# Kernel optimization log

Hardware: AMD Instinct MI355X
Metric: run time of the kernel (lower is better)

The kernel has to match this reference:

```python
import jax, jax.numpy as jnp
import numpy as np

B = 256          # batch
H = 1024         # conditioning_size (dec_hid_dim)
D = 256          # gst_dim
G = 32           # num_gst
C = 16           # num_cells
O = 256          # output_size


def setup_inputs() -> dict:
    key = jax.random.key(0)
    ks = jax.random.split(key, 7)
    hidden = jax.random.normal(ks[0], (B, H), dtype=jnp.float32)
    # per-cell embedding tables: nn.Embedding(num_gst, gst_dim) stacked over cells
    gst_emb = jax.random.normal(ks[1], (C, G, D), dtype=jnp.float32)
    # per-cell Linear(gst_dim + cond, cond): weight [H, H + D] (torch [out, in]), bias [H]
    attn_w = jax.random.normal(ks[2], (C, H, H + D), dtype=jnp.float32) * 0.02
    attn_b = jax.random.normal(ks[3], (C, H), dtype=jnp.float32) * 0.02
    # per-cell v: Parameter(torch.rand(cond))
    v = jax.random.uniform(ks[4], (C, H), dtype=jnp.float32)
    # out Linear(gst_dim, output_size)
    out_w = jax.random.normal(ks[5], (O, D), dtype=jnp.float32) * 0.02
    out_b = jax.random.normal(ks[6], (O,), dtype=jnp.float32) * 0.02
    return {"hidden": hidden, "gst_emb": gst_emb, "attn_w": attn_w,
            "attn_b": attn_b, "v": v, "out_w": out_w, "out_b": out_b}


def reference(hidden, gst_emb, attn_w, attn_b, v, out_w, out_b):
    # Original concatenates (hidden, encoder_outputs) along features; split the
    # linear weight accordingly instead of materializing the concat.
    w_hid = attn_w[:, :, :H]        # [C, H, H]
    w_enc = attn_w[:, :, H:]        # [C, H, D]
    # embedding lookup of arange(G) == the table rows themselves (same for all batch)
    enc = gst_emb                   # [C, G, D]
    hid_part = jnp.einsum('bh,coh->bco', hidden, w_hid)     # [B, C, Ho]
    enc_part = jnp.einsum('cgd,cod->cgo', enc, w_enc)       # [C, G, Ho]
    energy = jnp.tanh(hid_part[:, :, None, :] + enc_part[None]
                      + attn_b[None, :, None, :])           # [B, C, G, Ho]
    scores = jnp.einsum('bcgh,ch->bcg', energy, v)          # [B, C, G]
    attention = jax.nn.softmax(scores, axis=-1)             # softmax over num_gst
    weighted = jnp.einsum('bcg,cgd->bcd', attention, enc)   # [B, C, D]
    att_cat = attention.reshape(B, C * G)                   # torch.cat(att_list, dim=1)
    pooled = jnp.mean(weighted, axis=1)                     # [B, D]
    out = pooled @ out_w.T + out_b                          # [B, O]
    return (att_cat, out)
```

## Files before the change

kernel.cpp:

```cpp
#include <hip/hip_runtime.h>
#include <hip/hip_bf16.h>

#define B_  256
#define H_  1024
#define D_  256
#define G_  32
#define C_  16
#define O_  256
#define HD_ 1280
#define N1_ 16384

typedef __attribute__((ext_vector_type(8)))  short short8;
typedef __attribute__((ext_vector_type(4)))  short s16x4;
typedef __attribute__((ext_vector_type(4)))  float f32x4;
typedef __attribute__((ext_vector_type(16))) float f32x16;

#define MFMA32(a, b, c) __builtin_amdgcn_mfma_f32_32x32x16_bf16((a), (b), (c), 0, 0, 0)

__device__ __forceinline__ float tanh_c(float x) {
    float y = __expf(2.f * x);
    float t = 1.f - 2.f * __builtin_amdgcn_rcpf(y + 1.f);
    return fminf(fmaxf(t, -0.99999994f), 0.99999994f);
}

__device__ __forceinline__ short bfhi(float x) {
    return (short)(__float_as_uint(x) >> 16);
}
__device__ __forceinline__ short bflo(float x) {
    float fhi = __uint_as_float(__float_as_uint(x) & 0xFFFF0000u);
    return (short)(__float_as_uint(x - fhi) >> 16);
}

__device__ __forceinline__ void split4(const float4 v, s16x4& hi, s16x4& lo) {
    hi[0] = bfhi(v.x); lo[0] = bflo(v.x);
    hi[1] = bfhi(v.y); lo[1] = bflo(v.y);
    hi[2] = bfhi(v.z); lo[2] = bflo(v.z);
    hi[3] = bfhi(v.w); lo[3] = bflo(v.w);
}

__global__ __launch_bounds__(256, 2) void gemm1_kernel(
    const short* __restrict__ hidH, const short* __restrict__ hidL,
    const float* __restrict__ attn_w, const float* __restrict__ attn_b,
    float* __restrict__ hp)
{
    __shared__ float Bsf[4][32 * 32];

    const int tid  = threadIdx.x;
    const int wave = tid >> 6, lane = tid & 63;
    const int l31  = lane & 31;
    const int hi2  = (lane >> 5) * 2;
    const int sw   = l31 & 7;
    const int n0   = blockIdx.x * 32;

    f32x16 acc0, acc1;
    #pragma unroll
    for (int i = 0; i < 16; ++i) { acc0[i] = 0.f; acc1[i] = 0.f; }

    const int rS = tid >> 3;
    const int cS = (tid & 7) ^ (rS & 7);
    const float* pBsrc = attn_w + (size_t)(n0 + rS) * HD_ + cS * 4;

    const size_t aBase = (size_t)(wave * 2) * 32768 + (size_t)lane * 8;
    const short* pH0 = hidH + aBase;
    const short* pH1 = hidH + aBase + 32768;
    const short* pL0 = hidL + aBase;
    const short* pL1 = hidL + aBase + 32768;

    short8 aH0[2][2], aH1[2][2], aL0[2][2], aL1[2][2];

#define LOADA(SET, K)                                                         \
    {                                                                         \
        const int o_ = (K) * 1024;                                            \
        aH0[SET][0] = *(const short8*)(pH0 + o_);                             \
        aH0[SET][1] = *(const short8*)(pH0 + o_ + 512);                       \
        aH1[SET][0] = *(const short8*)(pH1 + o_);                             \
        aH1[SET][1] = *(const short8*)(pH1 + o_ + 512);                       \
        aL0[SET][0] = *(const short8*)(pL0 + o_);                             \
        aL0[SET][1] = *(const short8*)(pL0 + o_ + 512);                       \
        aL1[SET][0] = *(const short8*)(pL1 + o_);                             \
        aL1[SET][1] = *(const short8*)(pL1 + o_ + 512);                       \
    }

#define DMAB(BUF, K)                                                          \
    __builtin_amdgcn_global_load_lds(                                         \
        (const __attribute__((address_space(1))) void*)(pBsrc + (K) * 32),    \
        (__attribute__((address_space(3))) void*)(&Bsf[BUF][wave * 256]),     \
        16, 0, 0);

#define READB(BUF, KS, BH, BL)                                                \
    {                                                                         \
        const float* rp_ = &Bsf[BUF][l31 * 32];                               \
        const int kc_ = (KS) * 4 + hi2;                                       \
        float4 ca_ = *(const float4*)(rp_ + ((kc_    ) ^ sw) * 4);            \
        float4 cb_ = *(const float4*)(rp_ + ((kc_ + 1) ^ sw) * 4);            \
        s16x4 h0_, lo0_, h1_, lo1_;                                           \
        split4(ca_, h0_, lo0_);                                               \
        split4(cb_, h1_, lo1_);                                               \
        BH = short8{h0_[0],h0_[1],h0_[2],h0_[3],h1_[0],h1_[1],h1_[2],h1_[3]}; \
        BL = short8{lo0_[0],lo0_[1],lo0_[2],lo0_[3],                          \
                    lo1_[0],lo1_[1],lo1_[2],lo1_[3]};                         \
    }

#define ITER(P, K, VC, DOL, DODMA)                                            \
    {                                                                         \
        asm volatile("s_waitcnt vmcnt(" #VC ")" ::: "memory");                \
        __builtin_amdgcn_s_barrier();                                         \
        if (DOL) LOADA(P ^ 1, (K) + 1)                                        \
        __builtin_amdgcn_sched_barrier(0);                                    \
        if (DODMA) DMAB(((K) + 3) & 3, (K) + 3)                               \
        __builtin_amdgcn_sched_barrier(0);                                    \
        short8 bh0, bl0, bh1, bl1;                                            \
        READB((K) & 3, 0, bh0, bl0)                                           \
        READB((K) & 3, 1, bh1, bl1)                                           \
        __builtin_amdgcn_s_setprio(1);                                        \
        acc0 = MFMA32(aH0[P][0], bh0, acc0);                                  \
        acc1 = MFMA32(aH1[P][0], bh0, acc1);                                  \
        acc0 = MFMA32(aL0[P][0], bh0, acc0);                                  \
        acc1 = MFMA32(aL1[P][0], bh0, acc1);                                  \
        acc0 = MFMA32(aH0[P][0], bl0, acc0);                                  \
        acc1 = MFMA32(aH1[P][0], bl0, acc1);                                  \
        acc0 = MFMA32(aH0[P][1], bh1, acc0);                                  \
        acc1 = MFMA32(aH1[P][1], bh1, acc1);                                  \
        acc0 = MFMA32(aL0[P][1], bh1, acc0);                                  \
        acc1 = MFMA32(aL1[P][1], bh1, acc1);                                  \
        acc0 = MFMA32(aH0[P][1], bl1, acc0);                                  \
        acc1 = MFMA32(aH1[P][1], bl1, acc1);                                  \
        __builtin_amdgcn_s_setprio(0);                                        \
    }

    DMAB(0, 0)
    DMAB(1, 1)
    DMAB(2, 2)
    __builtin_amdgcn_sched_barrier(0);
    LOADA(0, 0)

    ITER(0, 0, 10, 1, 1)
    ITER(1, 1, 18, 1, 1)
    ITER(0, 2, 26, 1, 1)
    for (int k = 3; k <= 27; k += 2) {
        ITER(1, k,     18, 1, 1)
        ITER(0, k + 1, 18, 1, 1)
    }
    ITER(1, 29, 18, 1, 0)
    ITER(0, 30, 17, 1, 0)
    ITER(1, 31, 16, 0, 0)
#undef ITER
#undef READB
#undef DMAB
#undef LOADA

    const int col  = n0 + l31;
    const float bias = attn_b[col];
    const int rbase = wave * 64 + (lane >> 5) * 4;
    float* dcol = hp + col;
    #pragma unroll
    for (int r = 0; r < 16; ++r) {
        const int row = rbase + (r & 3) + 8 * (r >> 2);
        dcol[(size_t)row * N1_]        = tanh_c(acc0[r] + bias);
        dcol[(size_t)(row + 32) * N1_] = tanh_c(acc1[r] + bias);
    }
}

__global__ __launch_bounds__(256) void gemm2_kernel(
    const float* __restrict__ enc, const float* __restrict__ attn_w,
    const float* __restrict__ hidden, float* __restrict__ ep,
    short* __restrict__ hidH, short* __restrict__ hidL)
{
    const int tid  = threadIdx.x;
    const int wave = tid >> 6, lane = tid & 63;

    {
        const int bid = blockIdx.y * 16 + blockIdx.x;
        const int gid = bid * 256 + tid;
        if (gid < 32768) {
            const int s   = gid >> 12;
            const int k0  = (gid >> 7) & 31;
            const int ks  = (gid >> 6) & 1;
            const int ln  = gid & 63;
            const int row = s * 32 + (ln & 31);
            const int colk = k0 * 32 + ks * 16 + (ln >> 5) * 8;
            const float* src = hidden + (size_t)row * H_ + colk;
            s16x4 h0, l0, h1, l1;
            split4(*(const float4*)src, h0, l0);
            split4(*(const float4*)(src + 4), h1, l1);
            *(short8*)(hidH + (size_t)gid * 8) =
                short8{h0[0],h0[1],h0[2],h0[3],h1[0],h1[1],h1[2],h1[3]};
            *(short8*)(hidL + (size_t)gid * 8) =
                short8{l0[0],l0[1],l0[2],l0[3],l1[0],l1[1],l1[2],l1[3]};
        }
    }

    const int c  = blockIdx.y;
    const int n0 = blockIdx.x * 64 + wave * 16;
    const int l16 = lane & 15;
    const int lk  = (lane >> 4) * 8;

#define MFMA16(a, b, c) __builtin_amdgcn_mfma_f32_16x16x32_bf16((a), (b), (c), 0, 0, 0)
    f32x4 acc[2];
    acc[0] = f32x4{0.f, 0.f, 0.f, 0.f};
    acc[1] = f32x4{0.f, 0.f, 0.f, 0.f};

    const float* encp = enc + c * (G_ * D_);
    const float* wp   = attn_w + (size_t)c * H_ * HD_ + H_;

    #pragma unroll
    for (int kk = 0; kk < 8; ++kk) {
        const int k0 = kk * 32 + lk;
        short8 ah[2], al[2], bh, bl;
        #pragma unroll
        for (int mi = 0; mi < 2; ++mi) {
            const float* p = encp + (mi * 16 + l16) * D_ + k0;
            s16x4 h0, l0, h1, l1;
            split4(*(const float4*)p, h0, l0);
            split4(*(const float4*)(p + 4), h1, l1);
            ah[mi] = short8{h0[0],h0[1],h0[2],h0[3],h1[0],h1[1],h1[2],h1[3]};
            al[mi] = short8{l0[0],l0[1],l0[2],l0[3],l1[0],l1[1],l1[2],l1[3]};
        }
        {
            const float* p = wp + (size_t)(n0 + l16) * HD_ + k0;
            s16x4 h0, l0, h1, l1;
            split4(*(const float4*)p, h0, l0);
            split4(*(const float4*)(p + 4), h1, l1);
            bh = short8{h0[0],h0[1],h0[2],h0[3],h1[0],h1[1],h1[2],h1[3]};
            bl = short8{l0[0],l0[1],l0[2],l0[3],l1[0],l1[1],l1[2],l1[3]};
        }
        #pragma unroll
        for (int mi = 0; mi < 2; ++mi) {
            acc[mi] = MFMA16(ah[mi], bh, acc[mi]);
            acc[mi] = MFMA16(al[mi], bh, acc[mi]);
            acc[mi] = MFMA16(ah[mi], bl, acc[mi]);
        }
    }

    const int lr = (lane >> 4) * 4;
    #pragma unroll
    for (int mi = 0; mi < 2; ++mi) {
        const int g = mi * 16 + lr;
        const int o = n0 + l16;
        float* dst = ep + (c * G_ + g) * H_ + o;
        f32x4 vacc = acc[mi];
        dst[0]      = tanh_c(vacc[0]);
        dst[H_]     = tanh_c(vacc[1]);
        dst[2 * H_] = tanh_c(vacc[2]);
        dst[3 * H_] = tanh_c(vacc[3]);
    }
#undef MFMA16
}

__global__ __launch_bounds__(256) void attn_kernel(
    const float* __restrict__ hp, const float* __restrict__ ep,
    const float* __restrict__ v, const float* __restrict__ enc,
    float* __restrict__ out, float* __restrict__ wt)
{
    const int c  = blockIdx.x;
    const int b0 = blockIdx.y * 4;
    const int tid  = threadIdx.x;
    const int wave = tid >> 6, lane = tid & 63;

    __shared__ float s_att[4][G_];
    __shared__ float s_sc[4][G_];

    f32x4 vv[4], tav[4][4];
    const float* vrow = v + c * H_;
    #pragma unroll
    for (int j = 0; j < 4; ++j)
        vv[j] = *(const f32x4*)(vrow + lane * 4 + j * 256);
    #pragma unroll
    for (int bi = 0; bi < 4; ++bi) {
        const float* hprow = hp + (size_t)(b0 + bi) * N1_ + c * H_;
        #pragma unroll
        for (int j = 0; j < 4; ++j)
            tav[bi][j] = *(const f32x4*)(hprow + lane * 4 + j * 256);
    }

    #pragma unroll
    for (int gg = 0; gg < 8; ++gg) {
        const int g = wave * 8 + gg;
        const float* eprow = ep + (size_t)(c * G_ + g) * H_;
        float s[4] = {0.f, 0.f, 0.f, 0.f};
        #pragma unroll
        for (int j = 0; j < 4; ++j) {
            const f32x4 tb = *(const f32x4*)(eprow + lane * 4 + j * 256);
            #pragma unroll
            for (int e = 0; e < 4; ++e) {
                const float tbx = tb[e];
                const float w   = vv[j][e];
                #pragma unroll
                for (int bi = 0; bi < 4; ++bi) {
                    const float ta  = tav[bi][j][e];
                    const float num = ta + tbx;
                    const float den = fmaf(ta, tbx, 1.f);
                    s[bi] = fmaf(num * __builtin_amdgcn_rcpf(den), w, s[bi]);
                }
            }
        }
        #pragma unroll
        for (int off = 32; off > 0; off >>= 1) {
            s[0] += __shfl_down(s[0], off, 64);
            s[1] += __shfl_down(s[1], off, 64);
            s[2] += __shfl_down(s[2], off, 64);
            s[3] += __shfl_down(s[3], off, 64);
        }
        if (lane == 0) {
            s_sc[0][g] = s[0]; s_sc[1][g] = s[1];
            s_sc[2][g] = s[2]; s_sc[3][g] = s[3];
        }
    }
    __syncthreads();

    if (tid < 128) {
        const int bi = tid >> 5, g = tid & 31;
        float sv = s_sc[bi][g];
        float m = sv;
        #pragma unroll
        for (int off = 16; off > 0; off >>= 1)
            m = fmaxf(m, __shfl_xor(m, off, 32));
        const float e = __expf(sv - m);
        float sum = e;
        #pragma unroll
        for (int off = 16; off > 0; off >>= 1)
            sum += __shfl_xor(sum, off, 32);
        const float a = e / sum;
        s_att[bi][g] = a;
        out[(size_t)(b0 + bi) * (C_ * G_) + c * G_ + g] = a;
    }
    __syncthreads();

    float w0 = 0.f, w1 = 0.f, w2 = 0.f, w3 = 0.f;
    const float* encc = enc + c * (G_ * D_) + tid;
    #pragma unroll
    for (int g = 0; g < G_; ++g) {
        const float e = encc[g * D_];
        w0 = fmaf(s_att[0][g], e, w0);
        w1 = fmaf(s_att[1][g], e, w1);
        w2 = fmaf(s_att[2][g], e, w2);
        w3 = fmaf(s_att[3][g], e, w3);
    }
    wt[(size_t)((b0 + 0) * C_ + c) * D_ + tid] = w0;
    wt[(size_t)((b0 + 1) * C_ + c) * D_ + tid] = w1;
    wt[(size_t)((b0 + 2) * C_ + c) * D_ + tid] = w2;
    wt[(size_t)((b0 + 3) * C_ + c) * D_ + tid] = w3;
}

__global__ __launch_bounds__(256) void out_kernel(
    const float* __restrict__ wt, const float* __restrict__ out_w,
    const float* __restrict__ out_b, float* __restrict__ out)
{
    const int b = blockIdx.x, tid = threadIdx.x;
    __shared__ float pooled[D_];

    float s = 0.f;
    #pragma unroll
    for (int c = 0; c < C_; ++c)
        s += wt[(size_t)(b * C_ + c) * D_ + tid];
    pooled[tid] = s * (1.f / 16.f);
    __syncthreads();

    float acc = out_b[tid];
    const float* wrow = out_w + tid * D_;
    #pragma unroll 8
    for (int dc = 0; dc < 64; ++dc) {
        float4 w4 = *(const float4*)(wrow + dc * 4);
        acc += pooled[dc * 4 + 0] * w4.x;
        acc += pooled[dc * 4 + 1] * w4.y;
        acc += pooled[dc * 4 + 2] * w4.z;
        acc += pooled[dc * 4 + 3] * w4.w;
    }
    out[(size_t)B_ * (C_ * G_) + b * O_ + tid] = acc;
}

extern "C" void kernel_launch(void* const* d_in, const int* in_sizes, int n_in,
                              void* d_out, int out_size, void* d_ws, size_t ws_size,
                              hipStream_t stream) {
    const float* hidden = (const float*)d_in[0];
    const float* enc    = (const float*)d_in[1];
    const float* attn_w = (const float*)d_in[2];
    const float* attn_b = (const float*)d_in[3];
    const float* v      = (const float*)d_in[4];
    const float* out_w  = (const float*)d_in[5];
    const float* out_b  = (const float*)d_in[6];
    float* out = (float*)d_out;

    float* hp = (float*)d_ws;
    float* ep = hp + (size_t)B_ * N1_;
    float* wt = ep + (size_t)C_ * G_ * H_;
    short* hidH = (short*)(wt + (size_t)B_ * C_ * D_);
    short* hidL = hidH + (size_t)B_ * H_;

    gemm2_kernel<<<dim3(16, C_), 256, 0, stream>>>(enc, attn_w, hidden, ep, hidH, hidL);
    gemm1_kernel<<<512, 256, 0, stream>>>(hidH, hidL, attn_w, attn_b, hp);
    attn_kernel<<<dim3(C_, B_ / 4), 256, 0, stream>>>(hp, ep, v, enc, out, wt);
    out_kernel<<<B_, 256, 0, stream>>>(wt, out_w, out_b, out);
}
```

Before: 210.6 us.

## Split gemm1 across 8 waves with one 32-row accumulator each

Doubles the gemm1 block from 4 to 8 waves, so each wave owns one 32x32 output tile instead of two. Half the lanes issue the B-tile DMA into LDS, and the vmcnt wait counts in the software pipeline are retuned to the smaller per-wave load count. The aim is more waves per CU to hide latency and fewer registers per wave. The cost is half the A-fragment reuse across the two accumulators, more LDS reads of B per block, and heavier barrier synchronisation.

```diff
diff --git a/kernel.cpp b/kernel.cpp
--- a/kernel.cpp
+++ b/kernel.cpp
@@ -38,7 +38,7 @@
     hi[3] = bfhi(v.w); lo[3] = bflo(v.w);
 }
 
-__global__ __launch_bounds__(256, 2) void gemm1_kernel(
+__global__ __launch_bounds__(512, 4) void gemm1_kernel(
     const short* __restrict__ hidH, const short* __restrict__ hidL,
     const float* __restrict__ attn_w, const float* __restrict__ attn_b,
     float* __restrict__ hp)
@@ -52,40 +52,35 @@
     const int sw   = l31 & 7;
     const int n0   = blockIdx.x * 32;
 
-    f32x16 acc0, acc1;
-    #pragma unroll
-    for (int i = 0; i < 16; ++i) { acc0[i] = 0.f; acc1[i] = 0.f; }
-
-    const int rS = tid >> 3;
-    const int cS = (tid & 7) ^ (rS & 7);
-    const float* pBsrc = attn_w + (size_t)(n0 + rS) * HD_ + cS * 4;
-
-    const size_t aBase = (size_t)(wave * 2) * 32768 + (size_t)lane * 8;
-    const short* pH0 = hidH + aBase;
-    const short* pH1 = hidH + aBase + 32768;
-    const short* pL0 = hidL + aBase;
-    const short* pL1 = hidL + aBase + 32768;
-
-    short8 aH0[2][2], aH1[2][2], aL0[2][2], aL1[2][2];
+    f32x16 acc;
+    #pragma unroll
+    for (int i = 0; i < 16; ++i) acc[i] = 0.f;
+
+    const int rD = wave * 4 + (lane >> 3);
+    const int cD = (lane & 7) ^ (rD & 7);
+    const float* pBsrc = attn_w + (size_t)(n0 + rD) * HD_ + cD * 4;
+
+    const size_t aBase = (size_t)wave * 32768 + (size_t)lane * 8;
+    const short* pH = hidH + aBase;
+    const short* pL = hidL + aBase;
+
+    short8 aH[2][2], aL[2][2];
 
 #define LOADA(SET, K)                                                         \
     {                                                                         \
         const int o_ = (K) * 1024;                                            \
-        aH0[SET][0] = *(const short8*)(pH0 + o_);                             \
-        aH0[SET][1] = *(const short8*)(pH0 + o_ + 512);                       \
-        aH1[SET][0] = *(const short8*)(pH1 + o_);                             \
-        aH1[SET][1] = *(const short8*)(pH1 + o_ + 512);                       \
-        aL0[SET][0] = *(const short8*)(pL0 + o_);                             \
-        aL0[SET][1] = *(const short8*)(pL0 + o_ + 512);                       \
-        aL1[SET][0] = *(const short8*)(pL1 + o_);                             \
-        aL1[SET][1] = *(const short8*)(pL1 + o_ + 512);                       \
+        aH[SET][0] = *(const short8*)(pH + o_);                               \
+        aH[SET][1] = *(const short8*)(pH + o_ + 512);                         \
+        aL[SET][0] = *(const short8*)(pL + o_);                               \
+        aL[SET][1] = *(const short8*)(pL + o_ + 512);                         \
     }
 
 #define DMAB(BUF, K)                                                          \
-    __builtin_amdgcn_global_load_lds(                                         \
-        (const __attribute__((address_space(1))) void*)(pBsrc + (K) * 32),    \
-        (__attribute__((address_space(3))) void*)(&Bsf[BUF][wave * 256]),     \
-        16, 0, 0);
+    if (lane < 32)                                                            \
+        __builtin_amdgcn_global_load_lds(                                     \
+            (const __attribute__((address_space(1))) void*)(pBsrc + (K) * 32),\
+            (__attribute__((address_space(3))) void*)(&Bsf[BUF][wave * 128]), \
+            16, 0, 0);
 
 #define READB(BUF, KS, BH, BL)                                                \
     {                                                                         \
@@ -113,37 +108,30 @@
         READB((K) & 3, 0, bh0, bl0)                                           \
         READB((K) & 3, 1, bh1, bl1)                                           \
         __builtin_amdgcn_s_setprio(1);                                        \
-        acc0 = MFMA32(aH0[P][0], bh0, acc0);                                  \
-        acc1 = MFMA32(aH1[P][0], bh0, acc1);                                  \
-        acc0 = MFMA32(aL0[P][0], bh0, acc0);                                  \
-        acc1 = MFMA32(aL1[P][0], bh0, acc1);                                  \
-        acc0 = MFMA32(aH0[P][0], bl0, acc0);                                  \
-        acc1 = MFMA32(aH1[P][0], bl0, acc1);                                  \
-        acc0 = MFMA32(aH0[P][1], bh1, acc0);                                  \
-        acc1 = MFMA32(aH1[P][1], bh1, acc1);                                  \
-        acc0 = MFMA32(aL0[P][1], bh1, acc0);                                  \
-        acc1 = MFMA32(aL1[P][1], bh1, acc1);                                  \
-        acc0 = MFMA32(aH0[P][1], bl1, acc0);                                  \
-        acc1 = MFMA32(aH1[P][1], bl1, acc1);                                  \
+        acc = MFMA32(aH[P][0], bh0, acc);                                     \
+        acc = MFMA32(aL[P][0], bh0, acc);                                     \
+        acc = MFMA32(aH[P][0], bl0, acc);                                     \
+        acc = MFMA32(aH[P][1], bh1, acc);                                     \
+        acc = MFMA32(aL[P][1], bh1, acc);                                     \
+        acc = MFMA32(aH[P][1], bl1, acc);                                     \
         __builtin_amdgcn_s_setprio(0);                                        \
     }
 
     DMAB(0, 0)
+    __builtin_amdgcn_sched_barrier(0);
+    LOADA(0, 0)
+    __builtin_amdgcn_sched_barrier(0);
     DMAB(1, 1)
     DMAB(2, 2)
-    __builtin_amdgcn_sched_barrier(0);
-    LOADA(0, 0)
-
-    ITER(0, 0, 10, 1, 1)
-    ITER(1, 1, 18, 1, 1)
-    ITER(0, 2, 26, 1, 1)
-    for (int k = 3; k <= 27; k += 2) {
-        ITER(1, k,     18, 1, 1)
-        ITER(0, k + 1, 18, 1, 1)
-    }
-    ITER(1, 29, 18, 1, 0)
-    ITER(0, 30, 17, 1, 0)
-    ITER(1, 31, 16, 0, 0)
+
+    ITER(0, 0, 2, 1, 1)
+    for (int k = 1; k <= 27; k += 2) {
+        ITER(1, k,     1, 1, 1)
+        ITER(0, k + 1, 1, 1, 1)
+    }
+    ITER(1, 29, 1, 1, 0)
+    ITER(0, 30, 0, 1, 0)
+    ITER(1, 31, 0, 0, 0)
 #undef ITER
 #undef READB
 #undef DMAB
@@ -151,13 +139,12 @@
 
     const int col  = n0 + l31;
     const float bias = attn_b[col];
-    const int rbase = wave * 64 + (lane >> 5) * 4;
+    const int rbase = wave * 32 + (lane >> 5) * 4;
     float* dcol = hp + col;
     #pragma unroll
     for (int r = 0; r < 16; ++r) {
         const int row = rbase + (r & 3) + 8 * (r >> 2);
-        dcol[(size_t)row * N1_]        = tanh_c(acc0[r] + bias);
-        dcol[(size_t)(row + 32) * N1_] = tanh_c(acc1[r] + bias);
+        dcol[(size_t)row * N1_] = tanh_c(acc[r] + bias);
     }
 }
 
@@ -388,7 +375,7 @@
     short* hidL = hidH + (size_t)B_ * H_;
 
     gemm2_kernel<<<dim3(16, C_), 256, 0, stream>>>(enc, attn_w, hidden, ep, hidH, hidL);
-    gemm1_kernel<<<512, 256, 0, stream>>>(hidH, hidL, attn_w, attn_b, hp);
+    gemm1_kernel<<<512, 512, 0, stream>>>(hidH, hidL, attn_w, attn_b, hp);
     attn_kernel<<<dim3(C_, B_ / 4), 256, 0, stream>>>(hp, ep, v, enc, out, wt);
     out_kernel<<<B_, 256, 0, stream>>>(wt, out_w, out_b, out);
 }
```

New measurement: 211.3 us. No clear change (+0.3%).

## Retile gemm1 to 128x128 blocks with 8 waves sharing B tiles

Applied to the files above, without the earlier changes.

The hidden-projection GEMM moves from 512 blocks of 256 threads, each computing all 256 rows for a 32-column strip, to a 2x128 grid of 512-thread blocks, each computing a 128x128 tile. Each block now loads a 128-column B slice into LDS with two DMA loads per wave, and the eight waves split into 2 row groups by 4 column groups. Each B element is now fetched by two blocks instead of one, and each A element is reused across four column groups per block. The change also reorders the prologue loads, retunes the vmcnt wait counts, and quadruples the LDS buffer, which may limit occupancy.

```diff
diff --git a/kernel.cpp b/kernel.cpp
--- a/kernel.cpp
+++ b/kernel.cpp
@@ -38,29 +38,32 @@
     hi[3] = bfhi(v.w); lo[3] = bflo(v.w);
 }
 
-__global__ __launch_bounds__(256, 2) void gemm1_kernel(
+__global__ __launch_bounds__(512, 2) void gemm1_kernel(
     const short* __restrict__ hidH, const short* __restrict__ hidL,
     const float* __restrict__ attn_w, const float* __restrict__ attn_b,
     float* __restrict__ hp)
 {
-    __shared__ float Bsf[4][32 * 32];
+    __shared__ float Bsf[4][128 * 32];
 
     const int tid  = threadIdx.x;
     const int wave = tid >> 6, lane = tid & 63;
     const int l31  = lane & 31;
     const int hi2  = (lane >> 5) * 2;
     const int sw   = l31 & 7;
-    const int n0   = blockIdx.x * 32;
+    const int m0   = blockIdx.x * 128;
+    const int n0   = blockIdx.y * 128;
 
     f32x16 acc0, acc1;
     #pragma unroll
     for (int i = 0; i < 16; ++i) { acc0[i] = 0.f; acc1[i] = 0.f; }
 
-    const int rS = tid >> 3;
-    const int cS = (tid & 7) ^ (rS & 7);
-    const float* pBsrc = attn_w + (size_t)(n0 + rS) * HD_ + cS * 4;
-
-    const size_t aBase = (size_t)(wave * 2) * 32768 + (size_t)lane * 8;
+    const int rD = wave * 8 + (lane >> 3);
+    const int cD = (lane & 7) ^ (rD & 7);
+    const float* pBsrc0 = attn_w + (size_t)(n0 + rD) * HD_ + cD * 4;
+    const float* pBsrc1 = pBsrc0 + (size_t)64 * HD_;
+
+    const int s0 = blockIdx.x * 4 + (wave >> 2) * 2;
+    const size_t aBase = (size_t)s0 * 32768 + (size_t)lane * 8;
     const short* pH0 = hidH + aBase;
     const short* pH1 = hidH + aBase + 32768;
     const short* pL0 = hidL + aBase;
@@ -82,14 +85,20 @@
     }
 
 #define DMAB(BUF, K)                                                          \
-    __builtin_amdgcn_global_load_lds(                                         \
-        (const __attribute__((address_space(1))) void*)(pBsrc + (K) * 32),    \
-        (__attribute__((address_space(3))) void*)(&Bsf[BUF][wave * 256]),     \
-        16, 0, 0);
+    {                                                                         \
+        __builtin_amdgcn_global_load_lds(                                     \
+            (const __attribute__((address_space(1))) void*)(pBsrc0 + (K)*32), \
+            (__attribute__((address_space(3))) void*)(&Bsf[BUF][wave * 256]), \
+            16, 0, 0);                                                        \
+        __builtin_amdgcn_global_load_lds(                                     \
+            (const __attribute__((address_space(1))) void*)(pBsrc1 + (K)*32), \
+            (__attribute__((address_space(3))) void*)(&Bsf[BUF][2048 + wave * 256]), \
+            16, 0, 0);                                                        \
+    }
 
 #define READB(BUF, KS, BH, BL)                                                \
     {                                                                         \
-        const float* rp_ = &Bsf[BUF][l31 * 32];                               \
+        const float* rp_ = &Bsf[BUF][((wave & 3) * 32 + l31) * 32];           \
         const int kc_ = (KS) * 4 + hi2;                                       \
         float4 ca_ = *(const float4*)(rp_ + ((kc_    ) ^ sw) * 4);            \
         float4 cb_ = *(const float4*)(rp_ + ((kc_ + 1) ^ sw) * 4);            \
@@ -129,29 +138,28 @@
     }
 
     DMAB(0, 0)
+    __builtin_amdgcn_sched_barrier(0);
+    LOADA(0, 0)
+    __builtin_amdgcn_sched_barrier(0);
     DMAB(1, 1)
     DMAB(2, 2)
-    __builtin_amdgcn_sched_barrier(0);
-    LOADA(0, 0)
-
-    ITER(0, 0, 10, 1, 1)
-    ITER(1, 1, 18, 1, 1)
-    ITER(0, 2, 26, 1, 1)
-    for (int k = 3; k <= 27; k += 2) {
-        ITER(1, k,     18, 1, 1)
-        ITER(0, k + 1, 18, 1, 1)
-    }
-    ITER(1, 29, 18, 1, 0)
-    ITER(0, 30, 17, 1, 0)
-    ITER(1, 31, 16, 0, 0)
+
+    ITER(0, 0, 4, 1, 1)
+    for (int k = 1; k <= 27; k += 2) {
+        ITER(1, k,     2, 1, 1)
+        ITER(0, k + 1, 2, 1, 1)
+    }
+    ITER(1, 29, 2, 1, 0)
+    ITER(0, 30, 0, 1, 0)
+    ITER(1, 31, 0, 0, 0)
 #undef ITER
 #undef READB
 #undef DMAB
 #undef LOADA
 
-    const int col  = n0 + l31;
+    const int col  = n0 + (wave & 3) * 32 + l31;
     const float bias = attn_b[col];
-    const int rbase = wave * 64 + (lane >> 5) * 4;
+    const int rbase = m0 + (wave >> 2) * 64 + (lane >> 5) * 4;
     float* dcol = hp + col;
     #pragma unroll
     for (int r = 0; r < 16; ++r) {
@@ -388,7 +396,7 @@
     short* hidL = hidH + (size_t)B_ * H_;
 
     gemm2_kernel<<<dim3(16, C_), 256, 0, stream>>>(enc, attn_w, hidden, ep, hidH, hidL);
-    gemm1_kernel<<<512, 256, 0, stream>>>(hidH, hidL, attn_w, attn_b, hp);
+    gemm1_kernel<<<dim3(2, 128), 512, 0, stream>>>(hidH, hidL, attn_w, attn_b, hp);
     attn_kernel<<<dim3(C_, B_ / 4), 256, 0, stream>>>(hp, ep, v, enc, out, wt);
     out_kernel<<<B_, 256, 0, stream>>>(wt, out_w, out_b, out);
 }
```

After: 221.6 us. 1.05x slower.
